# Kernel tuning notes

Measured on AMD Instinct MI355X. Metric: run time of the kernel, lower is better.

The kernel has to match this reference:

```python
import jax, jax.numpy as jnp
import numpy as np

B, S, D, H, DK = 2, 2048, 1024, 16, 64  # batch, seq, d_model, heads, head_dim


def setup_inputs() -> dict:
    key = jax.random.key(0)
    ks = jax.random.split(key, 11)
    inp = {
        "v": jax.random.normal(ks[0], (B, S, D), dtype=jnp.float32),
        "k": jax.random.normal(ks[1], (B, S, D), dtype=jnp.float32),
        "q": jax.random.normal(ks[2], (B, S, D), dtype=jnp.float32),
        # per-head Linear(d_model, d_k): torch weight shape [d_k, d_model], stacked over heads
        "Wq": jax.random.normal(ks[3], (H, DK, D), dtype=jnp.float32) * 0.02,
        "bq": jax.random.normal(ks[4], (H, DK), dtype=jnp.float32) * 0.02,
        "Wk": jax.random.normal(ks[5], (H, DK, D), dtype=jnp.float32) * 0.02,
        "bk": jax.random.normal(ks[6], (H, DK), dtype=jnp.float32) * 0.02,
        "Wv": jax.random.normal(ks[7], (H, DK, D), dtype=jnp.float32) * 0.02,
        "bv": jax.random.normal(ks[8], (H, DK), dtype=jnp.float32) * 0.02,
        "Wo": jax.random.normal(ks[9], (D, D), dtype=jnp.float32) * 0.02,
        "bo": jax.random.normal(ks[10], (D,), dtype=jnp.float32) * 0.02,
    }
    return inp


def reference(v, k, q, Wq, bq, Wk, bk, Wv, bv, Wo, bo):
    # Batched per-head projections (original uses a python loop over h Linears).
    # torch Linear: y = x @ W.T + b  ->  einsum over last dim of W.
    q2 = jnp.einsum("bsd,hkd->bhsk", q, Wq) + bq[None, :, None, :]
    k2 = jnp.einsum("bsd,hkd->bhsk", k, Wk) + bk[None, :, None, :]
    v2 = jnp.einsum("bsd,hkd->bhsk", v, Wv) + bv[None, :, None, :]
    # FAITHFUL to source bug: attention(v2, k2, q2) -> scores from v2 @ k2^T,
    # softmax, then weighted sum of q2. (dropout = identity in eval mode)
    scores = jnp.einsum("bhsk,bhtk->bhst", v2, k2) / jnp.sqrt(jnp.float32(DK))
    attn = jax.nn.softmax(scores, axis=-1)
    out = jnp.einsum("bhst,bhtk->bhsk", attn, q2)
    # concat heads in order (head i -> slice [i*d_k:(i+1)*d_k])
    out = out.transpose(0, 2, 1, 3).reshape(B, S, H * DK)
    return out @ Wo.T + bo
```

## Files before the change

### kernel.cpp

```cpp
#include <hip/hip_runtime.h>
#include <stdint.h>

#define B_  2
#define S_  2048
#define D_  1024
#define H_  16
#define DK_ 64
#define VST 2176

typedef unsigned short u16;
typedef short bf16x8 __attribute__((ext_vector_type(8)));
typedef float f32x4  __attribute__((ext_vector_type(4)));

#define MFMA(a,b,c) __builtin_amdgcn_mfma_f32_16x16x32_bf16((a),(b),(c),0,0,0)
#define EXP2(x) __builtin_amdgcn_exp2f(x)

static __device__ __forceinline__ u16 f2bf(float f) {
    uint32_t u = __float_as_uint(f);
    u += 0x7fffu + ((u >> 16) & 1u);
    return (u16)(u >> 16);
}
static __device__ __forceinline__ uint32_t pk2(float x, float y) {
    return __builtin_amdgcn_perm(__float_as_uint(y) + 0x8000u,
                                 __float_as_uint(x) + 0x8000u, 0x07060302u);
}

typedef const __attribute__((address_space(1))) void* gas_p;
typedef __attribute__((address_space(3))) void* las_p;
static __device__ __forceinline__ void gld16(const void* g, void* l) {
    __builtin_amdgcn_global_load_lds((gas_p)g, (las_p)l, 16, 0, 0);
}


__global__ void conv_all(const float* __restrict__ v, const float* __restrict__ k,
                         const float* __restrict__ q,
                         const float* __restrict__ Wv, const float* __restrict__ Wk,
                         const float* __restrict__ Wq, const float* __restrict__ Wo,
                         u16* __restrict__ dst) {
    const int b = blockIdx.x;
    const float* s;
    size_t loc, segbase;
    if (b < 12288) {
        const int t = b >> 12;
        s = (t == 0) ? v : (t == 1 ? k : q);
        segbase = (size_t)t * 4194304;
        loc = (size_t)(b & 4095) * 1024;
    } else {
        const int t = (b - 12288) >> 10;
        s = (t == 0) ? Wv : (t == 1 ? Wk : (t == 2 ? Wq : Wo));
        segbase = 12582912 + (size_t)t * 1048576;
        loc = (size_t)(b & 1023) * 1024;
    }
    loc += threadIdx.x * 4;
    float4 f = *(const float4*)(s + loc);
    ushort4 o;
    o.x = f2bf(f.x); o.y = f2bf(f.y); o.z = f2bf(f.z); o.w = f2bf(f.w);
    *(ushort4*)(dst + segbase + loc) = o;
}


__global__ __launch_bounds__(256) void proj_gemm(
    const u16* __restrict__ Xb, const u16* __restrict__ Wb,
    const float* __restrict__ bv, const float* __restrict__ bk, const float* __restrict__ bq,
    u16* __restrict__ v2, u16* __restrict__ k2, u16* __restrict__ q2T)
{
    __shared__ alignas(16) char smem[40960];
    u16* lA = (u16*)smem;
    u16* lB = (u16*)(smem + 16384);
    u16* epi = (u16*)smem;

    const int z = blockIdx.z;
    const u16* A = Xb + (size_t)z * 4194304;
    const u16* W = Wb + (size_t)z * 1048576;
    const float* bias = (z == 0) ? bv : (z == 1 ? bk : bq);

    const int tid = threadIdx.x;
    const int lane = tid & 63, wave = tid >> 6;
    const int wm = wave >> 1, wn = wave & 1;
    const int q = lane >> 4, l15 = lane & 15;
    const int q4 = q * 4;

    const int f = blockIdx.y * 8 + blockIdx.x;
    const int rowbase = (f & 31) * 128;
    const int colbase = (f >> 5) * 128;

    const int srow = wave * 8 + (lane >> 3);
    const int cg = (lane & 7) ^ (lane >> 3);
    const u16* gA = A + (size_t)(rowbase + srow) * D_ + cg * 8;
    const u16* gW = W + (size_t)(colbase + srow) * D_ + cg * 8;
    u16* lAp = lA + wave * 512 + lane * 8;
    u16* lBp = lB + wave * 512 + lane * 8;

    const int sw = l15 & 7;
    const int fo0 = (q ^ sw) * 8;
    const int fo1 = fo0 ^ 32;

    f32x4 acc[4][4] = {};

    for (int k0 = 0; k0 < D_; k0 += 64) {
        #pragma unroll
        for (int j = 0; j < 4; j++) {
            gld16(gA + k0 + (size_t)j * 32 * D_, lAp + j * 2048);
            gld16(gW + k0 + (size_t)j * 32 * D_, lBp + j * 2048);
        }
        __syncthreads();
        bf16x8 a0[4], a1[4], b0[4], b1[4];
        #pragma unroll
        for (int mi = 0; mi < 4; mi++) {
            const int r = (wm * 64 + mi * 16 + l15) * 64;
            a0[mi] = *(const bf16x8*)&lA[r + fo0];
            a1[mi] = *(const bf16x8*)&lA[r + fo1];
        }
        #pragma unroll
        for (int ni = 0; ni < 4; ni++) {
            const int r = (wn * 64 + ni * 16 + l15) * 64;
            b0[ni] = *(const bf16x8*)&lB[r + fo0];
            b1[ni] = *(const bf16x8*)&lB[r + fo1];
        }
        #pragma unroll
        for (int mi = 0; mi < 4; mi++)
            #pragma unroll
            for (int ni = 0; ni < 4; ni++) {
                acc[mi][ni] = MFMA(a0[mi], b0[ni], acc[mi][ni]);
                acc[mi][ni] = MFMA(a1[mi], b1[ni], acc[mi][ni]);
            }
        __syncthreads();
    }

    u16* ep = epi + wave * (64 * 80);
    const int h = (colbase + wn * 64) >> 6;
    const int Mrow0 = rowbase + wm * 64;
    const int bb = Mrow0 >> 11;

    if (z < 2) {
        u16* outp = (z == 0) ? v2 : k2;
        const float scale = (z == 0) ? 0.18033688011112042f : 1.0f;
        #pragma unroll
        for (int mi = 0; mi < 4; mi++)
            #pragma unroll
            for (int ni = 0; ni < 4; ni++) {
                const float bc = bias[colbase + wn * 64 + ni * 16 + l15];
                #pragma unroll
                for (int rg = 0; rg < 4; rg++)
                    ep[(mi * 16 + q4 + rg) * 80 + ni * 16 + l15] =
                        f2bf((acc[mi][ni][rg] + bc) * scale);
            }
        asm volatile("s_waitcnt lgkmcnt(0)" ::: "memory");
        const int s = (Mrow0 + lane) & (S_ - 1);
        u16* gb = outp + ((size_t)(bb * H_ + h) * S_ + s) * DK_;
        #pragma unroll
        for (int j = 0; j < 8; j++)
            *(uint4*)(gb + j * 8) = *(const uint4*)&ep[lane * 80 + j * 8];
    } else {
        #pragma unroll
        for (int mi = 0; mi < 4; mi++)
            #pragma unroll
            for (int ni = 0; ni < 4; ni++) {
                const float bc = bias[colbase + wn * 64 + ni * 16 + l15];
                uint2 pk;
                pk.x = pk2(acc[mi][ni][0] + bc, acc[mi][ni][1] + bc);
                pk.y = pk2(acc[mi][ni][2] + bc, acc[mi][ni][3] + bc);
                *(uint2*)&ep[(ni * 16 + l15) * 80 + mi * 16 + q4] = pk;
            }
        asm volatile("s_waitcnt lgkmcnt(0)" ::: "memory");
        const int s0g = Mrow0 & (S_ - 1);
        u16* gb = q2T + ((size_t)(bb * H_ + h) * DK_ + lane) * VST + s0g;
        #pragma unroll
        for (int j = 0; j < 8; j++)
            *(uint4*)(gb + j * 8) = *(const uint4*)&ep[lane * 80 + j * 8];
    }
}


__global__ __launch_bounds__(512, 2) void flash_attn(
    const u16* __restrict__ v2, const u16* __restrict__ k2,
    const u16* __restrict__ q2T, u16* __restrict__ Ob)
{
    __shared__ alignas(16) char smem[82944];
    u16* lK   = (u16*)smem;
    u16* lV   = (u16*)(smem + 32768);
    u16* ldsP = (u16*)(smem + 65536);
    float* Xo = (float*)smem;
    float* Xl = (float*)(smem + 69632);

    const int tid = threadIdx.x;
    const int lane = tid & 63, wave = tid >> 6;
    const int th = wave >> 2, wl = wave & 3;
    const int q = lane >> 4, l15 = lane & 15;
    const int q4 = q * 4;
    const int bh = blockIdx.x & 31;
    const int sbase = (blockIdx.x >> 5) * 256;
    const int tbase = th * 1024;

    const u16* Qp = v2  + (size_t)bh * S_ * DK_;
    const u16* Kp = k2  + (size_t)bh * S_ * DK_;
    const u16* Vp = q2T + (size_t)bh * DK_ * VST;

    const int srow8 = lane >> 3;
    const int cs    = lane & 7;
    const int cg    = cs ^ srow8;
    const int krow0 = wl * 16 + srow8;
    u16* lKh = lK + th * 8192;
    u16* lVh = lV + th * 8192;

    bf16x8 bq[4][2];
    #pragma unroll
    for (int g = 0; g < 4; g++) {
        const u16* qp = Qp + (size_t)(sbase + wl * 64 + g * 16 + l15) * DK_ + q * 8;
        bq[g][0] = *(const bf16x8*)(qp);
        bq[g][1] = *(const bf16x8*)(qp + 32);
    }

    bf16x8 ones;
    #pragma unroll
    for (int i = 0; i < 8; i++) ones[i] = (short)0x3F80;

    f32x4 o_acc[4][4] = {};
    f32x4 o_l[4] = {};

    const int sw = l15 & 7;
    const int fc0 = (q ^ sw) * 8;
    const int fc1 = fc0 ^ 32;

    {
        const u16* kg = Kp + (size_t)(tbase + krow0) * DK_ + cg * 8;
        const u16* vg = Vp + (size_t)krow0 * VST + tbase + cg * 8;
        u16* lkd = lKh + wl * 1024 + lane * 8;
        u16* lvd = lVh + wl * 1024 + lane * 8;
        gld16(kg, lkd);
        gld16(kg + 8 * DK_, lkd + 512);
        gld16(vg, lvd);
        gld16(vg + (size_t)8 * VST, lvd + 512);
    }

    u16* Pw = ldsP + wave * (16 * 68);

    for (int it = 0; it < 16; ++it) {
        const int buf = it & 1;
        __syncthreads();
        if (it + 1 < 16) {
            const int t1 = tbase + (it + 1) * 64;
            const u16* kg = Kp + (size_t)(t1 + krow0) * DK_ + cg * 8;
            const u16* vg = Vp + (size_t)krow0 * VST + t1 + cg * 8;
            u16* lkd = lKh + (buf ^ 1) * 4096 + wl * 1024 + lane * 8;
            u16* lvd = lVh + (buf ^ 1) * 4096 + wl * 1024 + lane * 8;
            gld16(kg, lkd);
            gld16(kg + 8 * DK_, lkd + 512);
            gld16(vg, lvd);
            gld16(vg + (size_t)8 * VST, lvd + 512);
        }

        const u16* Kt = lKh + buf * 4096;
        const u16* Vt = lVh + buf * 4096;
        bf16x8 ak0[4], ak1[4], av0[4], av1[4];
        #pragma unroll
        for (int mi = 0; mi < 4; mi++) {
            const int r = (mi * 16 + l15) * 64;
            ak0[mi] = *(const bf16x8*)&Kt[r + fc0];
            ak1[mi] = *(const bf16x8*)&Kt[r + fc1];
            av0[mi] = *(const bf16x8*)&Vt[r + fc0];
            av1[mi] = *(const bf16x8*)&Vt[r + fc1];
        }

        #pragma unroll
        for (int g = 0; g < 4; g++) {
            f32x4 sa[4];
            #pragma unroll
            for (int mi = 0; mi < 4; mi++) {
                f32x4 zz = {};
                zz = MFMA(ak0[mi], bq[g][0], zz);
                sa[mi] = MFMA(ak1[mi], bq[g][1], zz);
            }
            #pragma unroll
            for (int mi = 0; mi < 4; mi++) {
                float p0 = EXP2(sa[mi][0]);
                float p1 = EXP2(sa[mi][1]);
                float p2 = EXP2(sa[mi][2]);
                float p3 = EXP2(sa[mi][3]);
                uint2 pk;
                pk.x = __builtin_amdgcn_perm(__float_as_uint(p1), __float_as_uint(p0), 0x07060302u);
                pk.y = __builtin_amdgcn_perm(__float_as_uint(p3), __float_as_uint(p2), 0x07060302u);
                *(uint2*)&Pw[l15 * 68 + mi * 16 + q4] = pk;
            }
            asm volatile("s_waitcnt lgkmcnt(0)" ::: "memory");
            bf16x8 bp0, bp1;
            {
                uint2* r0 = (uint2*)&bp0;
                r0[0] = *(const uint2*)&Pw[l15 * 68 + q * 8];
                r0[1] = *(const uint2*)&Pw[l15 * 68 + q * 8 + 4];
                uint2* r1 = (uint2*)&bp1;
                r1[0] = *(const uint2*)&Pw[l15 * 68 + 32 + q * 8];
                r1[1] = *(const uint2*)&Pw[l15 * 68 + 32 + q * 8 + 4];
            }
            #pragma unroll
            for (int mi = 0; mi < 4; mi++) {
                o_acc[g][mi] = MFMA(av0[mi], bp0, o_acc[g][mi]);
                o_acc[g][mi] = MFMA(av1[mi], bp1, o_acc[g][mi]);
            }
            o_l[g] = MFMA(ones, bp0, o_l[g]);
            o_l[g] = MFMA(ones, bp1, o_l[g]);
        }
    }

    __syncthreads();
    if (th == 1) {
        #pragma unroll
        for (int g = 0; g < 4; g++) {
            const int sr = wl * 64 + g * 16 + l15;
            #pragma unroll
            for (int mi = 0; mi < 4; mi++)
                *(f32x4*)&Xo[sr * 68 + mi * 16 + q4] = o_acc[g][mi];
            if (q == 0) Xl[sr] = o_l[g][0];
        }
    }
    __syncthreads();
    if (th == 0) {
        const int bb = bh >> 4, h = bh & 15;
        #pragma unroll
        for (int g = 0; g < 4; g++) {
            const int sr = wl * 64 + g * 16 + l15;
            const float inv_l = 1.0f / (o_l[g][0] + Xl[sr]);
            const int s = sbase + sr;
            #pragma unroll
            for (int mi = 0; mi < 4; mi++) {
                f32x4 p = *(const f32x4*)&Xo[sr * 68 + mi * 16 + q4];
                ushort4 o4;
                o4.x = f2bf((o_acc[g][mi][0] + p[0]) * inv_l);
                o4.y = f2bf((o_acc[g][mi][1] + p[1]) * inv_l);
                o4.z = f2bf((o_acc[g][mi][2] + p[2]) * inv_l);
                o4.w = f2bf((o_acc[g][mi][3] + p[3]) * inv_l);
                *(ushort4*)(Ob + (size_t)(bb * S_ + s) * (H_ * DK_) + h * DK_ + mi * 16 + q4) = o4;
            }
        }
    }
}


__global__ __launch_bounds__(256) void out_gemm(
    const u16* __restrict__ Ob, const u16* __restrict__ Wob,
    const float* __restrict__ bo, float* __restrict__ out)
{
    __shared__ alignas(16) u16 lA[128 * 64];
    __shared__ alignas(16) u16 lB[64 * 64];

    const int tid = threadIdx.x;
    const int lane = tid & 63, wave = tid >> 6;
    const int wm = wave >> 1, wn = wave & 1;
    const int q = lane >> 4, l15 = lane & 15;
    const int q4 = q * 4;

    const int f = blockIdx.y * 16 + blockIdx.x;
    const int rowbase = (f & 31) * 128;
    const int colbase = (f >> 5) * 64;

    const int srow = wave * 8 + (lane >> 3);
    const int cg = (lane & 7) ^ (lane >> 3);
    const u16* gA = Ob  + (size_t)(rowbase + srow) * D_ + cg * 8;
    const u16* gW = Wob + (size_t)(colbase + srow) * D_ + cg * 8;
    u16* lAp = lA + wave * 512 + lane * 8;
    u16* lBp = lB + wave * 512 + lane * 8;

    const int sw = l15 & 7;
    const int fo0 = (q ^ sw) * 8;
    const int fo1 = fo0 ^ 32;

    f32x4 acc[4][2] = {};

    for (int k0 = 0; k0 < D_; k0 += 64) {
        #pragma unroll
        for (int j = 0; j < 4; j++)
            gld16(gA + k0 + (size_t)j * 32 * D_, lAp + j * 2048);
        #pragma unroll
        for (int j = 0; j < 2; j++)
            gld16(gW + k0 + (size_t)j * 32 * D_, lBp + j * 2048);
        __syncthreads();
        bf16x8 a0[4], a1[4], b0[2], b1[2];
        #pragma unroll
        for (int mi = 0; mi < 4; mi++) {
            const int r = (wm * 64 + mi * 16 + l15) * 64;
            a0[mi] = *(const bf16x8*)&lA[r + fo0];
            a1[mi] = *(const bf16x8*)&lA[r + fo1];
        }
        #pragma unroll
        for (int ni = 0; ni < 2; ni++) {
            const int r = (wn * 32 + ni * 16 + l15) * 64;
            b0[ni] = *(const bf16x8*)&lB[r + fo0];
            b1[ni] = *(const bf16x8*)&lB[r + fo1];
        }
        #pragma unroll
        for (int mi = 0; mi < 4; mi++)
            #pragma unroll
            for (int ni = 0; ni < 2; ni++) {
                acc[mi][ni] = MFMA(a0[mi], b0[ni], acc[mi][ni]);
                acc[mi][ni] = MFMA(a1[mi], b1[ni], acc[mi][ni]);
            }
        __syncthreads();
    }

    #pragma unroll
    for (int mi = 0; mi < 4; mi++)
        #pragma unroll
        for (int ni = 0; ni < 2; ni++) {
            const int c = colbase + wn * 32 + ni * 16 + l15;
            const float bc = bo[c];
            #pragma unroll
            for (int rg = 0; rg < 4; rg++) {
                const int r = rowbase + wm * 64 + mi * 16 + q4 + rg;
                out[(size_t)r * D_ + c] = acc[mi][ni][rg] + bc;
            }
        }
}


extern "C" void kernel_launch(void* const* d_in, const int* in_sizes, int n_in,
                              void* d_out, int out_size, void* d_ws, size_t ws_size,
                              hipStream_t stream) {
    const float* v  = (const float*)d_in[0];
    const float* k  = (const float*)d_in[1];
    const float* qq = (const float*)d_in[2];
    const float* Wq = (const float*)d_in[3];
    const float* bq = (const float*)d_in[4];
    const float* Wk = (const float*)d_in[5];
    const float* bk = (const float*)d_in[6];
    const float* Wv = (const float*)d_in[7];
    const float* bv = (const float*)d_in[8];
    const float* Wo = (const float*)d_in[9];
    const float* bo = (const float*)d_in[10];
    float* out = (float*)d_out;

    char* w = (char*)d_ws;
    u16* cvtb = (u16*)w;
    u16* v2  = (u16*)(w + 33554432);
    u16* k2  = (u16*)(w + 41943040);
    u16* q2T = (u16*)(w + 50331648);
    u16* Ob  = (u16*)(w + 59244544);

    conv_all<<<16384, 256, 0, stream>>>(v, k, qq, Wv, Wk, Wq, Wo, cvtb);
    proj_gemm<<<dim3(8, 32, 3), 256, 0, stream>>>(cvtb, cvtb + 12582912,
                                                  bv, bk, bq, v2, k2, q2T);
    flash_attn<<<256, 512, 0, stream>>>(v2, k2, q2T, Ob);
    out_gemm<<<dim3(16, 32), 256, 0, stream>>>(Ob, cvtb + 15728640, bo, out);
}
```

Measured before the change: 216.7 us.

## Double-buffer LDS tiles in projection and output GEMMs with K-step 32

Both the QKV projection GEMM and the output GEMM switch from single-buffered 64-wide K tiles to double-buffered 32-wide K tiles. The next tile's global-to-LDS loads are issued before the MFMAs on the current tile, so load latency overlaps compute and only one barrier is needed per iteration. The swizzle is changed to a 4-chunk XOR pattern for the narrower rows. The trade-off is twice as many loop iterations, barriers and smaller load batches per step.

```diff
diff --git a/kernel.cpp b/kernel.cpp
--- a/kernel.cpp
+++ b/kernel.cpp
@@ -84,48 +84,46 @@
     const int rowbase = (f & 31) * 128;
     const int colbase = (f >> 5) * 128;
 
-    const int srow = wave * 8 + (lane >> 3);
-    const int cg = (lane & 7) ^ (lane >> 3);
+    const int srow = wave * 16 + (lane >> 2);
+    const int cg = (lane & 3) ^ ((lane >> 2) & 3);
     const u16* gA = A + (size_t)(rowbase + srow) * D_ + cg * 8;
     const u16* gW = W + (size_t)(colbase + srow) * D_ + cg * 8;
-    u16* lAp = lA + wave * 512 + lane * 8;
-    u16* lBp = lB + wave * 512 + lane * 8;
-
-    const int sw = l15 & 7;
-    const int fo0 = (q ^ sw) * 8;
-    const int fo1 = fo0 ^ 32;
+    const int sdst = wave * 512 + lane * 8;
+
+    const int fo0 = (q ^ (l15 & 3)) * 8;
 
     f32x4 acc[4][4] = {};
 
-    for (int k0 = 0; k0 < D_; k0 += 64) {
-        #pragma unroll
-        for (int j = 0; j < 4; j++) {
-            gld16(gA + k0 + (size_t)j * 32 * D_, lAp + j * 2048);
-            gld16(gW + k0 + (size_t)j * 32 * D_, lBp + j * 2048);
-        }
+    gld16(gA,           lA + sdst);
+    gld16(gA + 64 * D_, lA + 2048 + sdst);
+    gld16(gW,           lB + sdst);
+    gld16(gW + 64 * D_, lB + 2048 + sdst);
+
+    for (int it = 0; it < 32; ++it) {
+        const int buf = it & 1;
         __syncthreads();
-        bf16x8 a0[4], a1[4], b0[4], b1[4];
-        #pragma unroll
-        for (int mi = 0; mi < 4; mi++) {
-            const int r = (wm * 64 + mi * 16 + l15) * 64;
-            a0[mi] = *(const bf16x8*)&lA[r + fo0];
-            a1[mi] = *(const bf16x8*)&lA[r + fo1];
-        }
-        #pragma unroll
-        for (int ni = 0; ni < 4; ni++) {
-            const int r = (wn * 64 + ni * 16 + l15) * 64;
-            b0[ni] = *(const bf16x8*)&lB[r + fo0];
-            b1[ni] = *(const bf16x8*)&lB[r + fo1];
-        }
-        #pragma unroll
-        for (int mi = 0; mi < 4; mi++)
-            #pragma unroll
-            for (int ni = 0; ni < 4; ni++) {
-                acc[mi][ni] = MFMA(a0[mi], b0[ni], acc[mi][ni]);
-                acc[mi][ni] = MFMA(a1[mi], b1[ni], acc[mi][ni]);
-            }
-        __syncthreads();
-    }
+        if (it + 1 < 32) {
+            const int k1 = (it + 1) * 32;
+            const int ob = (buf ^ 1) * 4096;
+            gld16(gA + k1,           lA + ob + sdst);
+            gld16(gA + k1 + 64 * D_, lA + ob + 2048 + sdst);
+            gld16(gW + k1,           lB + ob + sdst);
+            gld16(gW + k1 + 64 * D_, lB + ob + 2048 + sdst);
+        }
+        bf16x8 af[4], bfr[4];
+        #pragma unroll
+        for (int mi = 0; mi < 4; mi++)
+            af[mi] = *(const bf16x8*)&lA[buf * 4096 + (wm * 64 + mi * 16 + l15) * 32 + fo0];
+        #pragma unroll
+        for (int ni = 0; ni < 4; ni++)
+            bfr[ni] = *(const bf16x8*)&lB[buf * 4096 + (wn * 64 + ni * 16 + l15) * 32 + fo0];
+        #pragma unroll
+        for (int mi = 0; mi < 4; mi++)
+            #pragma unroll
+            for (int ni = 0; ni < 4; ni++)
+                acc[mi][ni] = MFMA(af[mi], bfr[ni], acc[mi][ni]);
+    }
+    __syncthreads();
 
     u16* ep = epi + wave * (64 * 80);
     const int h = (colbase + wn * 64) >> 6;
@@ -340,8 +338,8 @@
     const u16* __restrict__ Ob, const u16* __restrict__ Wob,
     const float* __restrict__ bo, float* __restrict__ out)
 {
-    __shared__ alignas(16) u16 lA[128 * 64];
-    __shared__ alignas(16) u16 lB[64 * 64];
+    __shared__ alignas(16) u16 lA[2][128 * 32];
+    __shared__ alignas(16) u16 lB[2][64 * 32];
 
     const int tid = threadIdx.x;
     const int lane = tid & 63, wave = tid >> 6;
@@ -353,48 +351,41 @@
     const int rowbase = (f & 31) * 128;
     const int colbase = (f >> 5) * 64;
 
-    const int srow = wave * 8 + (lane >> 3);
-    const int cg = (lane & 7) ^ (lane >> 3);
+    const int srow = wave * 16 + (lane >> 2);
+    const int cg = (lane & 3) ^ ((lane >> 2) & 3);
     const u16* gA = Ob  + (size_t)(rowbase + srow) * D_ + cg * 8;
     const u16* gW = Wob + (size_t)(colbase + srow) * D_ + cg * 8;
-    u16* lAp = lA + wave * 512 + lane * 8;
-    u16* lBp = lB + wave * 512 + lane * 8;
-
-    const int sw = l15 & 7;
-    const int fo0 = (q ^ sw) * 8;
-    const int fo1 = fo0 ^ 32;
+    const int sdst = wave * 512 + lane * 8;
+
+    const int fo0 = (q ^ (l15 & 3)) * 8;
 
     f32x4 acc[4][2] = {};
 
-    for (int k0 = 0; k0 < D_; k0 += 64) {
-        #pragma unroll
-        for (int j = 0; j < 4; j++)
-            gld16(gA + k0 + (size_t)j * 32 * D_, lAp + j * 2048);
-        #pragma unroll
-        for (int j = 0; j < 2; j++)
-            gld16(gW + k0 + (size_t)j * 32 * D_, lBp + j * 2048);
+    gld16(gA,           &lA[0][sdst]);
+    gld16(gA + 64 * D_, &lA[0][2048 + sdst]);
+    gld16(gW,           &lB[0][sdst]);
+
+    for (int it = 0; it < 32; ++it) {
+        const int buf = it & 1;
         __syncthreads();
-        bf16x8 a0[4], a1[4], b0[2], b1[2];
-        #pragma unroll
-        for (int mi = 0; mi < 4; mi++) {
-            const int r = (wm * 64 + mi * 16 + l15) * 64;
-            a0[mi] = *(const bf16x8*)&lA[r + fo0];
-            a1[mi] = *(const bf16x8*)&lA[r + fo1];
-        }
-        #pragma unroll
-        for (int ni = 0; ni < 2; ni++) {
-            const int r = (wn * 32 + ni * 16 + l15) * 64;
-            b0[ni] = *(const bf16x8*)&lB[r + fo0];
-            b1[ni] = *(const bf16x8*)&lB[r + fo1];
-        }
-        #pragma unroll
-        for (int mi = 0; mi < 4; mi++)
-            #pragma unroll
-            for (int ni = 0; ni < 2; ni++) {
-                acc[mi][ni] = MFMA(a0[mi], b0[ni], acc[mi][ni]);
-                acc[mi][ni] = MFMA(a1[mi], b1[ni], acc[mi][ni]);
-            }
-        __syncthreads();
+        if (it + 1 < 32) {
+            const int k1 = (it + 1) * 32;
+            gld16(gA + k1,           &lA[buf ^ 1][sdst]);
+            gld16(gA + k1 + 64 * D_, &lA[buf ^ 1][2048 + sdst]);
+            gld16(gW + k1,           &lB[buf ^ 1][sdst]);
+        }
+        bf16x8 af[4], bfr[2];
+        #pragma unroll
+        for (int mi = 0; mi < 4; mi++)
+            af[mi] = *(const bf16x8*)&lA[buf][(wm * 64 + mi * 16 + l15) * 32 + fo0];
+        #pragma unroll
+        for (int ni = 0; ni < 2; ni++)
+            bfr[ni] = *(const bf16x8*)&lB[buf][(wn * 32 + ni * 16 + l15) * 32 + fo0];
+        #pragma unroll
+        for (int mi = 0; mi < 4; mi++)
+            #pragma unroll
+            for (int ni = 0; ni < 2; ni++)
+                acc[mi][ni] = MFMA(af[mi], bfr[ni], acc[mi][ni]);
     }
 
     #pragma unroll
```

New measurement: 220.0 us. Within noise of the previous version (+1.5%).
